# Performance work log

Measured on AMD Instinct MI355X. Metric: run time of the kernel, lower is better.

The kernel has to match this reference:

```python
import jax, jax.numpy as jnp
import numpy as np

B, F_NODES, E = 1024, 128, 1024   # graphs, nodes/graph, edges/graph
H, HEADS = 128, 4
HD = H // HEADS


def setup_inputs() -> dict:
    key = jax.random.key(0)
    ks = jax.random.split(key, 24)
    f32 = jnp.float32
    n = jax.random.normal
    d = {
        "x": n(ks[0], (B, F_NODES), f32),
        "edge_index": jax.random.randint(ks[1], (2, E), 0, F_NODES, dtype=jnp.int32),
        # input projection Linear(1, H)
        "w_in": n(ks[2], (1, H), f32) * 0.5,
        "b_in": n(ks[3], (H,), f32) * 0.02,
        # GAT layer 0: heads=4, concat=True, per-head dim HD
        "gat0_w": n(ks[4], (H, H), f32) * (1.0 / np.sqrt(H)),
        "gat0_as": n(ks[5], (HEADS, HD), f32) * 0.1,
        "gat0_ad": n(ks[6], (HEADS, HD), f32) * 0.1,
        "gat0_b": n(ks[7], (H,), f32) * 0.02,
        "bn0_g": 1.0 + 0.1 * n(ks[8], (H,), f32),
        "bn0_b": 0.1 * n(ks[9], (H,), f32),
        "bn0_m": 0.1 * n(ks[10], (H,), f32),
        "bn0_v": 1.0 + 0.1 * jax.random.uniform(ks[11], (H,), f32),
        # GAT layer 1: heads=1, concat=False
        "gat1_w": n(ks[12], (H, H), f32) * (1.0 / np.sqrt(H)),
        "gat1_as": n(ks[13], (1, H), f32) * 0.1,
        "gat1_ad": n(ks[14], (1, H), f32) * 0.1,
        "gat1_b": n(ks[15], (H,), f32) * 0.02,
        "bn1_g": 1.0 + 0.1 * n(ks[16], (H,), f32),
        "bn1_b": 0.1 * n(ks[17], (H,), f32),
        "bn1_m": 0.1 * n(ks[18], (H,), f32),
        "bn1_v": 1.0 + 0.1 * jax.random.uniform(ks[19], (H,), f32),
        # classifier MLP H -> H//2 -> 1
        "w1": n(ks[20], (H, H // 2), f32) * (1.0 / np.sqrt(H)),
        "b1": n(ks[21], (H // 2,), f32) * 0.02,
        "w2": n(ks[22], (H // 2, 1), f32) * (1.0 / np.sqrt(H // 2)),
        "b2": n(ks[23], (1,), f32) * 0.02,
    }
    return d


def _gat(h, src, dst, N, W, a_s, a_d, b, concat):
    # PyG GATConv (shared lin for src/dst, leaky_relu slope 0.2, softmax over dst)
    heads, hd = a_s.shape
    xh = (h @ W).reshape(N, heads, hd)                      # [N, heads, hd]
    e = jax.nn.leaky_relu(
        jnp.sum(xh * a_s[None], -1)[src] + jnp.sum(xh * a_d[None], -1)[dst],
        0.2,
    )                                                        # [Etot, heads]
    m = jax.ops.segment_max(e, dst, num_segments=N)
    ex = jnp.exp(e - m[dst])
    s = jax.ops.segment_sum(ex, dst, num_segments=N)
    alpha = ex / s[dst]
    out = jax.ops.segment_sum(xh[src] * alpha[..., None], dst, num_segments=N)
    out = out.reshape(N, heads * hd) if concat else out[:, 0]
    return out + b


def _bn(h, g, b, m, v):
    return (h - m) / jnp.sqrt(v + 1e-5) * g + b


def reference(x, edge_index, w_in, b_in,
              gat0_w, gat0_as, gat0_ad, gat0_b, bn0_g, bn0_b, bn0_m, bn0_v,
              gat1_w, gat1_as, gat1_ad, gat1_b, bn1_g, bn1_b, bn1_m, bn1_v,
              w1, b1, w2, b2):
    Bsz, Fn = x.shape
    N = Bsz * Fn
    h = jax.nn.relu(x.reshape(N, 1) @ w_in + b_in)           # [N, H]
    # replicate per-graph edges with node offsets, then add self loops
    offs = jnp.arange(Bsz, dtype=edge_index.dtype) * Fn
    eib = (edge_index[:, None, :] + offs[None, :, None]).reshape(2, -1)
    loops = jnp.arange(N, dtype=edge_index.dtype)
    src = jnp.concatenate([eib[0], loops])
    dst = jnp.concatenate([eib[1], loops])
    h = _gat(h, src, dst, N, gat0_w, gat0_as, gat0_ad, gat0_b, True)
    h = jax.nn.relu(_bn(h, bn0_g, bn0_b, bn0_m, bn0_v))
    h = _gat(h, src, dst, N, gat1_w, gat1_as, gat1_ad, gat1_b, False)
    h = jax.nn.relu(_bn(h, bn1_g, bn1_b, bn1_m, bn1_v))
    # global mean pool (each graph has exactly Fn nodes)
    hp = h.reshape(Bsz, Fn, -1).mean(axis=1)                 # [B, H]
    z = jax.nn.relu(hp @ w1 + b1)
    return z @ w2 + b2                                       # [B, 1]
```

## Files before the change

### kernel.cpp

```cpp
#include <hip/hip_runtime.h>

#define FN   128
#define HDIM 128
#define NH   4
#define HSZ  32
#define EB   1024
#define ET   1152
#define RSW  132

typedef __attribute__((ext_vector_type(8))) short bf16x8;
typedef __attribute__((ext_vector_type(4))) float f32x4;
typedef unsigned int u32;
typedef unsigned short u16;

union U8 { bf16x8 v; u32 u[4]; };

__device__ __forceinline__ u32 pack_hl(float v) {
  const u32 u = __float_as_uint(v);
  const u32 hib = u & 0xFFFF0000u;
  const float lo = v - __uint_as_float(hib);
  return hib | (__float_as_uint(lo) >> 16);
}
__device__ __forceinline__ float unpack_val(u32 p) {
  return __uint_as_float(p & 0xFFFF0000u) + __uint_as_float(p << 16);
}

__device__ __forceinline__ void unpack_frag(const u32* __restrict__ q,
                                            bf16x8& hi, bf16x8& lo)
{
  const uint4 p0 = *(const uint4*)(q);
  const uint4 p1 = *(const uint4*)(q + 4);
  U8 H, L;
  H.u[0] = (p0.x >> 16) | (p0.y & 0xFFFF0000u);
  L.u[0] = (p0.x & 0xFFFFu) | (p0.y << 16);
  H.u[1] = (p0.z >> 16) | (p0.w & 0xFFFF0000u);
  L.u[1] = (p0.z & 0xFFFFu) | (p0.w << 16);
  H.u[2] = (p1.x >> 16) | (p1.y & 0xFFFF0000u);
  L.u[2] = (p1.x & 0xFFFFu) | (p1.y << 16);
  H.u[3] = (p1.z >> 16) | (p1.w & 0xFFFF0000u);
  L.u[3] = (p1.z & 0xFFFFu) | (p1.w << 16);
  hi = H.v; lo = L.v;
}

__device__ __forceinline__ void mfma_gemm(const u32* __restrict__ shl,
                                          float* __restrict__ sg,
                                          const float* __restrict__ W, int t)
{
  const int w = t >> 6, lane = t & 63;
  const int cg = w & 3, rh = w >> 2;
  const int m = lane & 15, quad = lane >> 4;
  const int n0 = cg * 32;

  f32x4 acc[2][2];
  #pragma unroll
  for (int s = 0; s < 2; ++s)
    #pragma unroll
    for (int ct = 0; ct < 2; ++ct) acc[s][ct] = (f32x4){0.f, 0.f, 0.f, 0.f};

  const u32* ap0 = shl + (rh * 32 + m) * RSW + quad * 8;
  const u32* ap1 = shl + (rh * 32 + 16 + m) * RSW + quad * 8;

  #pragma unroll
  for (int kc = 0; kc < 4; ++kc) {
    bf16x8 bhi[2], blo[2];
    #pragma unroll
    for (int ct = 0; ct < 2; ++ct) {
      const int n = n0 + ct * 16 + m;
      float wv[8];
      #pragma unroll
      for (int j = 0; j < 8; ++j) wv[j] = W[(kc * 32 + quad * 8 + j) * HDIM + n];
      U8 Hh, Ll;
      #pragma unroll
      for (int p = 0; p < 4; ++p) {
        const u32 u0 = __float_as_uint(wv[2 * p]);
        const u32 u1 = __float_as_uint(wv[2 * p + 1]);
        const u32 h0 = u0 & 0xFFFF0000u, h1 = u1 & 0xFFFF0000u;
        const float l0 = wv[2 * p]     - __uint_as_float(h0);
        const float l1 = wv[2 * p + 1] - __uint_as_float(h1);
        Hh.u[p] = (u0 >> 16) | h1;
        Ll.u[p] = (__float_as_uint(l0) >> 16) | (__float_as_uint(l1) & 0xFFFF0000u);
      }
      bhi[ct] = Hh.v; blo[ct] = Ll.v;
    }
    bf16x8 a0hi, a0lo, a1hi, a1lo;
    unpack_frag(ap0 + kc * 32, a0hi, a0lo);
    unpack_frag(ap1 + kc * 32, a1hi, a1lo);
    #pragma unroll
    for (int ct = 0; ct < 2; ++ct) {
      acc[0][ct] = __builtin_amdgcn_mfma_f32_16x16x32_bf16(a0hi, bhi[ct], acc[0][ct], 0, 0, 0);
      acc[0][ct] = __builtin_amdgcn_mfma_f32_16x16x32_bf16(a0lo, bhi[ct], acc[0][ct], 0, 0, 0);
      acc[0][ct] = __builtin_amdgcn_mfma_f32_16x16x32_bf16(a0hi, blo[ct], acc[0][ct], 0, 0, 0);
      acc[1][ct] = __builtin_amdgcn_mfma_f32_16x16x32_bf16(a1hi, bhi[ct], acc[1][ct], 0, 0, 0);
      acc[1][ct] = __builtin_amdgcn_mfma_f32_16x16x32_bf16(a1lo, bhi[ct], acc[1][ct], 0, 0, 0);
      acc[1][ct] = __builtin_amdgcn_mfma_f32_16x16x32_bf16(a1hi, blo[ct], acc[1][ct], 0, 0, 0);
    }
  }
  #pragma unroll
  for (int s = 0; s < 2; ++s) {
    const int row0 = rh * 32 + s * 16 + quad * 4;
    #pragma unroll
    for (int ct = 0; ct < 2; ++ct)
      #pragma unroll
      for (int r = 0; r < 4; ++r)
        sg[(row0 + r) * RSW + n0 + ct * 16 + m] = acc[s][ct][r];
  }
}

__global__ __launch_bounds__(1024) void gnn_fused_kernel(
    const float* __restrict__ x, const int* __restrict__ ei,
    const float* __restrict__ w_in, const float* __restrict__ b_in,
    const float* __restrict__ g0w, const float* __restrict__ g0as,
    const float* __restrict__ g0ad, const float* __restrict__ g0b,
    const float* __restrict__ bn0g, const float* __restrict__ bn0b,
    const float* __restrict__ bn0m, const float* __restrict__ bn0v,
    const float* __restrict__ g1w, const float* __restrict__ g1as,
    const float* __restrict__ g1ad, const float* __restrict__ g1b,
    const float* __restrict__ bn1g, const float* __restrict__ bn1b,
    const float* __restrict__ bn1m, const float* __restrict__ bn1v,
    const float* __restrict__ w1, const float* __restrict__ b1,
    const float* __restrict__ w2, const float* __restrict__ b2,
    float* __restrict__ out)
{
  __shared__ u32   shl[FN * RSW];
  __shared__ float sg[FN * RSW];
  __shared__ float s_alpha[NH * ET];
  __shared__ int   s_src[ET];
  __shared__ int   s_rp[FN + 1];
  __shared__ float s_es[512];
  __shared__ float s_ed[512];

  const int t = threadIdx.x;
  const int b = blockIdx.x;

  int* s_deg  = (int*)s_alpha;
  int* s_fill = s_deg + 128;
  const int e_dst = ei[EB + t];
  const int e_src = ei[t];
  if (t < 2 * FN) s_deg[t] = 0;
  __syncthreads();
  atomicAdd(&s_deg[e_dst], 1);

  {
    const int j = t & 127, q = t >> 7;
    const float wv = w_in[j], bv = b_in[j];
    for (int n = q * 16; n < q * 16 + 16; ++n) {
      const float v = fmaxf(fmaf(x[(size_t)b * FN + n], wv, bv), 0.f);
      shl[n * RSW + j] = pack_hl(v);
    }
  }
  __syncthreads();
  if (t < 64) {
    const int v0 = s_deg[2 * t] + 1, v1 = s_deg[2 * t + 1] + 1;
    const int p = v0 + v1;
    int sc = p;
    #pragma unroll
    for (int off = 1; off < 64; off <<= 1) {
      const int o = __shfl_up(sc, off, 64);
      if (t >= off) sc += o;
    }
    s_rp[2 * t] = sc - p;
    s_rp[2 * t + 1] = sc - v1;
    if (t == 63) s_rp[128] = sc;
  }
  __syncthreads();
  {
    const int p = s_rp[e_dst] + atomicAdd(&s_fill[e_dst], 1);
    s_src[p] = e_src;
  }
  if (t < FN) s_src[s_rp[t + 1] - 1] = t;
  __syncthreads();

  mfma_gemm(shl, sg, g0w, t);
  __syncthreads();

  if (t < 512) {
    const int hh = t >> 7, n = t & 127;
    const float* row = sg + n * RSW + hh * HSZ;
    float accs = 0.f, accd = 0.f;
    #pragma unroll
    for (int s = 0; s < 8; ++s) {
      const int d = ((n + s) & 7) * 4;
      const float4 v  = *(const float4*)(row + d);
      const float4 as = *(const float4*)(g0as + hh * HSZ + d);
      const float4 ad = *(const float4*)(g0ad + hh * HSZ + d);
      accs += v.x*as.x + v.y*as.y + v.z*as.z + v.w*as.w;
      accd += v.x*ad.x + v.y*ad.y + v.z*ad.z + v.w*ad.w;
    }
    s_es[hh * 128 + n] = accs;
    s_ed[hh * 128 + n] = accd;
  }
  __syncthreads();

  if (t < 512) {
    const int hh = t >> 7, n = t & 127;
    const float edv = s_ed[hh * 128 + n];
    const int e0 = s_rp[n], e1 = s_rp[n + 1];
    float mv = -1e30f;
    int e = e0;
    for (; e + 2 <= e1; e += 2) {
      const int sA = s_src[e], sB = s_src[e + 1];
      float vA = s_es[hh * 128 + sA] + edv;
      float vB = s_es[hh * 128 + sB] + edv;
      vA = (vA > 0.f) ? vA : 0.2f * vA;
      vB = (vB > 0.f) ? vB : 0.2f * vB;
      s_alpha[hh * ET + e] = vA;
      s_alpha[hh * ET + e + 1] = vB;
      mv = fmaxf(mv, fmaxf(vA, vB));
    }
    if (e < e1) {
      float vA = s_es[hh * 128 + s_src[e]] + edv;
      vA = (vA > 0.f) ? vA : 0.2f * vA;
      s_alpha[hh * ET + e] = vA;
      mv = fmaxf(mv, vA);
    }
    float sum = 0.f;
    e = e0;
    for (; e + 2 <= e1; e += 2) {
      const float exA = __expf(s_alpha[hh * ET + e] - mv);
      const float exB = __expf(s_alpha[hh * ET + e + 1] - mv);
      s_alpha[hh * ET + e] = exA;
      s_alpha[hh * ET + e + 1] = exB;
      sum += exA + exB;
    }
    if (e < e1) {
      const float exA = __expf(s_alpha[hh * ET + e] - mv);
      s_alpha[hh * ET + e] = exA;
      sum += exA;
    }
    s_ed[hh * 128 + n] = 1.f / sum;
  }
  __syncthreads();

  {
    const int cg = t & 15, rg = t >> 4;
    const int c0 = cg * 4, c1 = 64 + cg * 4;
    const int hhA = cg >> 3, hhB = 2 + (cg >> 3);
    const float4 bbA = *(const float4*)&g0b[c0],  bbB = *(const float4*)&g0b[c1];
    const float4 bmA = *(const float4*)&bn0m[c0], bmB = *(const float4*)&bn0m[c1];
    const float4 bvA = *(const float4*)&bn0v[c0], bvB = *(const float4*)&bn0v[c1];
    const float4 bgA = *(const float4*)&bn0g[c0], bgB = *(const float4*)&bn0g[c1];
    const float4 btA = *(const float4*)&bn0b[c0], btB = *(const float4*)&bn0b[c1];
    const float g0_ = bgA.x * rsqrtf(bvA.x + 1e-5f), g1_ = bgA.y * rsqrtf(bvA.y + 1e-5f);
    const float g2_ = bgA.z * rsqrtf(bvA.z + 1e-5f), g3_ = bgA.w * rsqrtf(bvA.w + 1e-5f);
    const float g4_ = bgB.x * rsqrtf(bvB.x + 1e-5f), g5_ = bgB.y * rsqrtf(bvB.y + 1e-5f);
    const float g6_ = bgB.z * rsqrtf(bvB.z + 1e-5f), g7_ = bgB.w * rsqrtf(bvB.w + 1e-5f);
    #pragma unroll
    for (int h2 = 0; h2 < 2; ++h2) {
      const int n = rg + h2 * 64;
      const int e0 = s_rp[n], e1 = s_rp[n + 1];
      const float rsvA = s_ed[hhA * 128 + n];
      const float rsvB = s_ed[hhB * 128 + n];
      float4 a0 = make_float4(0.f, 0.f, 0.f, 0.f);
      float4 a1 = make_float4(0.f, 0.f, 0.f, 0.f);
      for (int e = e0; e < e1; ++e) {
        const int s = s_src[e];
        const float alA = s_alpha[hhA * ET + e];
        const float alB = s_alpha[hhB * ET + e];
        const float4 v0 = *(const float4*)(sg + s * RSW + c0);
        const float4 v1 = *(const float4*)(sg + s * RSW + c1);
        a0.x = fmaf(alA, v0.x, a0.x); a0.y = fmaf(alA, v0.y, a0.y);
        a0.z = fmaf(alA, v0.z, a0.z); a0.w = fmaf(alA, v0.w, a0.w);
        a1.x = fmaf(alB, v1.x, a1.x); a1.y = fmaf(alB, v1.y, a1.y);
        a1.z = fmaf(alB, v1.z, a1.z); a1.w = fmaf(alB, v1.w, a1.w);
      }
      uint4 p0, p1;
      p0.x = pack_hl(fmaxf((a0.x * rsvA + bbA.x - bmA.x) * g0_ + btA.x, 0.f));
      p0.y = pack_hl(fmaxf((a0.y * rsvA + bbA.y - bmA.y) * g1_ + btA.y, 0.f));
      p0.z = pack_hl(fmaxf((a0.z * rsvA + bbA.z - bmA.z) * g2_ + btA.z, 0.f));
      p0.w = pack_hl(fmaxf((a0.w * rsvA + bbA.w - bmA.w) * g3_ + btA.w, 0.f));
      p1.x = pack_hl(fmaxf((a1.x * rsvB + bbB.x - bmB.x) * g4_ + btB.x, 0.f));
      p1.y = pack_hl(fmaxf((a1.y * rsvB + bbB.y - bmB.y) * g5_ + btB.y, 0.f));
      p1.z = pack_hl(fmaxf((a1.z * rsvB + bbB.z - bmB.z) * g6_ + btB.z, 0.f));
      p1.w = pack_hl(fmaxf((a1.w * rsvB + bbB.w - bmB.w) * g7_ + btB.w, 0.f));
      *(uint4*)(shl + n * RSW + c0) = p0;
      *(uint4*)(shl + n * RSW + c1) = p1;
    }
  }
  __syncthreads();

  mfma_gemm(shl, sg, g1w, t);
  __syncthreads();

  if (t < FN) {
    const int n = t;
    const float* row = sg + n * RSW;
    float accs = 0.f, accd = 0.f;
    #pragma unroll 8
    for (int s = 0; s < 32; ++s) {
      const int d = ((n + s) & 31) * 4;
      const float4 v  = *(const float4*)(row + d);
      const float4 as = *(const float4*)(g1as + d);
      const float4 ad = *(const float4*)(g1ad + d);
      accs += v.x*as.x + v.y*as.y + v.z*as.z + v.w*as.w;
      accd += v.x*ad.x + v.y*ad.y + v.z*ad.z + v.w*ad.w;
    }
    s_es[n] = accs;
    s_ed[n] = accd;
  }
  __syncthreads();

  if (t < FN) {
    const int n = t;
    const float edv = s_ed[n];
    const int e0 = s_rp[n], e1 = s_rp[n + 1];
    float mv = -1e30f;
    int e = e0;
    for (; e + 2 <= e1; e += 2) {
      const int sA = s_src[e], sB = s_src[e + 1];
      float vA = s_es[sA] + edv;
      float vB = s_es[sB] + edv;
      vA = (vA > 0.f) ? vA : 0.2f * vA;
      vB = (vB > 0.f) ? vB : 0.2f * vB;
      s_alpha[e] = vA;
      s_alpha[e + 1] = vB;
      mv = fmaxf(mv, fmaxf(vA, vB));
    }
    if (e < e1) {
      float vA = s_es[s_src[e]] + edv;
      vA = (vA > 0.f) ? vA : 0.2f * vA;
      s_alpha[e] = vA;
      mv = fmaxf(mv, vA);
    }
    float sum = 0.f;
    e = e0;
    for (; e + 2 <= e1; e += 2) {
      const float exA = __expf(s_alpha[e] - mv);
      const float exB = __expf(s_alpha[e + 1] - mv);
      s_alpha[e] = exA;
      s_alpha[e + 1] = exB;
      sum += exA + exB;
    }
    if (e < e1) {
      const float exA = __expf(s_alpha[e] - mv);
      s_alpha[e] = exA;
      sum += exA;
    }
    s_ed[n] = 1.f / sum;
  }
  __syncthreads();

  {
    const int cg = t & 15, rg = t >> 4;
    const int c0 = cg * 4, c1 = 64 + cg * 4;
    const float4 bbA = *(const float4*)&g1b[c0],  bbB = *(const float4*)&g1b[c1];
    const float4 bmA = *(const float4*)&bn1m[c0], bmB = *(const float4*)&bn1m[c1];
    const float4 bvA = *(const float4*)&bn1v[c0], bvB = *(const float4*)&bn1v[c1];
    const float4 bgA = *(const float4*)&bn1g[c0], bgB = *(const float4*)&bn1g[c1];
    const float4 btA = *(const float4*)&bn1b[c0], btB = *(const float4*)&bn1b[c1];
    const float g0_ = bgA.x * rsqrtf(bvA.x + 1e-5f), g1_ = bgA.y * rsqrtf(bvA.y + 1e-5f);
    const float g2_ = bgA.z * rsqrtf(bvA.z + 1e-5f), g3_ = bgA.w * rsqrtf(bvA.w + 1e-5f);
    const float g4_ = bgB.x * rsqrtf(bvB.x + 1e-5f), g5_ = bgB.y * rsqrtf(bvB.y + 1e-5f);
    const float g6_ = bgB.z * rsqrtf(bvB.z + 1e-5f), g7_ = bgB.w * rsqrtf(bvB.w + 1e-5f);
    #pragma unroll
    for (int h2 = 0; h2 < 2; ++h2) {
      const int n = rg + h2 * 64;
      const int e0 = s_rp[n], e1 = s_rp[n + 1];
      const float rsv = s_ed[n];
      float4 a0 = make_float4(0.f, 0.f, 0.f, 0.f);
      float4 a1 = make_float4(0.f, 0.f, 0.f, 0.f);
      for (int e = e0; e < e1; ++e) {
        const int s = s_src[e];
        const float al = s_alpha[e];
        const float4 v0 = *(const float4*)(sg + s * RSW + c0);
        const float4 v1 = *(const float4*)(sg + s * RSW + c1);
        a0.x = fmaf(al, v0.x, a0.x); a0.y = fmaf(al, v0.y, a0.y);
        a0.z = fmaf(al, v0.z, a0.z); a0.w = fmaf(al, v0.w, a0.w);
        a1.x = fmaf(al, v1.x, a1.x); a1.y = fmaf(al, v1.y, a1.y);
        a1.z = fmaf(al, v1.z, a1.z); a1.w = fmaf(al, v1.w, a1.w);
      }
      uint4 p0, p1;
      p0.x = pack_hl(fmaxf((a0.x * rsv + bbA.x - bmA.x) * g0_ + btA.x, 0.f));
      p0.y = pack_hl(fmaxf((a0.y * rsv + bbA.y - bmA.y) * g1_ + btA.y, 0.f));
      p0.z = pack_hl(fmaxf((a0.z * rsv + bbA.z - bmA.z) * g2_ + btA.z, 0.f));
      p0.w = pack_hl(fmaxf((a0.w * rsv + bbA.w - bmA.w) * g3_ + btA.w, 0.f));
      p1.x = pack_hl(fmaxf((a1.x * rsv + bbB.x - bmB.x) * g4_ + btB.x, 0.f));
      p1.y = pack_hl(fmaxf((a1.y * rsv + bbB.y - bmB.y) * g5_ + btB.y, 0.f));
      p1.z = pack_hl(fmaxf((a1.z * rsv + bbB.z - bmB.z) * g6_ + btB.z, 0.f));
      p1.w = pack_hl(fmaxf((a1.w * rsv + bbB.w - bmB.w) * g7_ + btB.w, 0.f));
      *(uint4*)(shl + n * RSW + c0) = p0;
      *(uint4*)(shl + n * RSW + c1) = p1;
    }
  }
  __syncthreads();

  float* s_red = s_alpha;
  {
    const int j = t & 127, q = t >> 7;
    float p = 0.f;
    for (int n = q * 16; n < q * 16 + 16; ++n) p += unpack_val(shl[n * RSW + j]);
    s_red[q * 128 + j] = p;
  }
  __syncthreads();
  if (t < FN) {
    float p = 0.f;
    #pragma unroll
    for (int q = 0; q < 8; ++q) p += s_red[q * 128 + t];
    s_es[t] = p * (1.f / 128.f);
  }
  __syncthreads();
  if (t < 512) {
    const int j = t & 63, part = t >> 6;
    float a = 0.f;
    #pragma unroll
    for (int k = part * 16; k < part * 16 + 16; ++k)
      a = fmaf(s_es[k], w1[k * 64 + j], a);
    s_ed[part * 64 + j] = a;
  }
  __syncthreads();
  if (t < 64) {
    float a = b1[t];
    #pragma unroll
    for (int p = 0; p < 8; ++p) a += s_ed[p * 64 + t];
    a = fmaxf(a, 0.f);
    float v = a * w2[t];
    #pragma unroll
    for (int off = 32; off > 0; off >>= 1) v += __shfl_down(v, off, 64);
    if (t == 0) out[b] = v + b2[0];
  }
}

extern "C" void kernel_launch(void* const* d_in, const int* in_sizes, int n_in,
                              void* d_out, int out_size, void* d_ws, size_t ws_size,
                              hipStream_t stream)
{
  const float* x    = (const float*)d_in[0];
  const int*   ei   = (const int*)d_in[1];
  const float* w_in = (const float*)d_in[2];
  const float* b_in = (const float*)d_in[3];
  const float* g0w  = (const float*)d_in[4];
  const float* g0as = (const float*)d_in[5];
  const float* g0ad = (const float*)d_in[6];
  const float* g0b  = (const float*)d_in[7];
  const float* bn0g = (const float*)d_in[8];
  const float* bn0b = (const float*)d_in[9];
  const float* bn0m = (const float*)d_in[10];
  const float* bn0v = (const float*)d_in[11];
  const float* g1w  = (const float*)d_in[12];
  const float* g1as = (const float*)d_in[13];
  const float* g1ad = (const float*)d_in[14];
  const float* g1b  = (const float*)d_in[15];
  const float* bn1g = (const float*)d_in[16];
  const float* bn1b = (const float*)d_in[17];
  const float* bn1m = (const float*)d_in[18];
  const float* bn1v = (const float*)d_in[19];
  const float* w1   = (const float*)d_in[20];
  const float* b1   = (const float*)d_in[21];
  const float* w2   = (const float*)d_in[22];
  const float* b2   = (const float*)d_in[23];

  gnn_fused_kernel<<<1024, 1024, 0, stream>>>(x, ei, w_in, b_in,
      g0w, g0as, g0ad, g0b, bn0g, bn0b, bn0m, bn0v,
      g1w, g1as, g1ad, g1b, bn1g, bn1b, bn1m, bn1v,
      w1, b1, w2, b2, (float*)d_out);
}
```

Measured before the change: 214.0 us.

## Fuse attention logits into GEMM epilogue and parallelize edge softmax without max

Attention logit dot products are now computed directly from MFMA accumulators with cross-lane shuffles, so the separate pass that re-read the projected features from shared memory goes away. Edge scores are computed and exponentiated in parallel over all edges, with the destination packed into the source index. The per-node serial max/exp/sum loops are replaced by a sum folded into the aggregation loop. Dropping the max subtraction risks overflow in exp when logits are large.

Result: slower. 226.5 us (+5.8%).

```diff
diff --git a/kernel.cpp b/kernel.cpp
--- a/kernel.cpp
+++ b/kernel.cpp
@@ -11,7 +11,6 @@
 typedef __attribute__((ext_vector_type(8))) short bf16x8;
 typedef __attribute__((ext_vector_type(4))) float f32x4;
 typedef unsigned int u32;
-typedef unsigned short u16;
 
 union U8 { bf16x8 v; u32 u[4]; };
 
@@ -42,16 +41,31 @@
   hi = H.v; lo = L.v;
 }
 
-__device__ __forceinline__ void mfma_gemm(const u32* __restrict__ shl,
-                                          float* __restrict__ sg,
-                                          const float* __restrict__ W, int t)
+__device__ __forceinline__ void split8(const float* w, bf16x8& hi, bf16x8& lo)
+{
+  U8 H, L;
+  #pragma unroll
+  for (int p = 0; p < 4; ++p) {
+    const u32 u0 = __float_as_uint(w[2 * p]);
+    const u32 u1 = __float_as_uint(w[2 * p + 1]);
+    const u32 h0 = u0 & 0xFFFF0000u, h1 = u1 & 0xFFFF0000u;
+    const float l0 = w[2 * p]     - __uint_as_float(h0);
+    const float l1 = w[2 * p + 1] - __uint_as_float(h1);
+    H.u[p] = (u0 >> 16) | h1;
+    L.u[p] = (__float_as_uint(l0) >> 16) | (__float_as_uint(l1) & 0xFFFF0000u);
+  }
+  hi = H.v; lo = L.v;
+}
+
+__device__ __forceinline__ void mfma_gemm_acc(const u32* __restrict__ shl,
+                                              const float* __restrict__ W,
+                                              int t, f32x4 acc[2][2])
 {
   const int w = t >> 6, lane = t & 63;
   const int cg = w & 3, rh = w >> 2;
   const int m = lane & 15, quad = lane >> 4;
   const int n0 = cg * 32;
 
-  f32x4 acc[2][2];
   #pragma unroll
   for (int s = 0; s < 2; ++s)
     #pragma unroll
@@ -69,18 +83,7 @@
       float wv[8];
       #pragma unroll
       for (int j = 0; j < 8; ++j) wv[j] = W[(kc * 32 + quad * 8 + j) * HDIM + n];
-      U8 Hh, Ll;
-      #pragma unroll
-      for (int p = 0; p < 4; ++p) {
-        const u32 u0 = __float_as_uint(wv[2 * p]);
-        const u32 u1 = __float_as_uint(wv[2 * p + 1]);
-        const u32 h0 = u0 & 0xFFFF0000u, h1 = u1 & 0xFFFF0000u;
-        const float l0 = wv[2 * p]     - __uint_as_float(h0);
-        const float l1 = wv[2 * p + 1] - __uint_as_float(h1);
-        Hh.u[p] = (u0 >> 16) | h1;
-        Ll.u[p] = (__float_as_uint(l0) >> 16) | (__float_as_uint(l1) & 0xFFFF0000u);
-      }
-      bhi[ct] = Hh.v; blo[ct] = Ll.v;
+      split8(wv, bhi[ct], blo[ct]);
     }
     bf16x8 a0hi, a0lo, a1hi, a1lo;
     unpack_frag(ap0 + kc * 32, a0hi, a0lo);
@@ -95,6 +98,14 @@
       acc[1][ct] = __builtin_amdgcn_mfma_f32_16x16x32_bf16(a1hi, blo[ct], acc[1][ct], 0, 0, 0);
     }
   }
+}
+
+__device__ __forceinline__ void store_acc(float* __restrict__ sg, int t,
+                                          const f32x4 acc[2][2])
+{
+  const int w = t >> 6, lane = t & 63;
+  const int cg = w & 3, rh = w >> 2;
+  const int m = lane & 15, quad = lane >> 4;
   #pragma unroll
   for (int s = 0; s < 2; ++s) {
     const int row0 = rh * 32 + s * 16 + quad * 4;
@@ -102,7 +113,45 @@
     for (int ct = 0; ct < 2; ++ct)
       #pragma unroll
       for (int r = 0; r < 4; ++r)
-        sg[(row0 + r) * RSW + n0 + ct * 16 + m] = acc[s][ct][r];
+        sg[(row0 + r) * RSW + cg * 32 + ct * 16 + m] = acc[s][ct][r];
+  }
+}
+
+__device__ __forceinline__ void wave_logits(const float* __restrict__ as_,
+                                            const float* __restrict__ ad_,
+                                            float* __restrict__ es,
+                                            float* __restrict__ ed,
+                                            int t, const f32x4 acc[2][2])
+{
+  const int w = t >> 6, lane = t & 63;
+  const int cg = w & 3, rh = w >> 2;
+  const int li = lane & 15, quad = lane >> 4;
+  const float was0 = as_[cg * 32 + li],      wad0 = ad_[cg * 32 + li];
+  const float was1 = as_[cg * 32 + 16 + li], wad1 = ad_[cg * 32 + 16 + li];
+  float pes[8], ped[8];
+  #pragma unroll
+  for (int s = 0; s < 2; ++s)
+    #pragma unroll
+    for (int r = 0; r < 4; ++r) {
+      pes[s * 4 + r] = acc[s][0][r] * was0 + acc[s][1][r] * was1;
+      ped[s * 4 + r] = acc[s][0][r] * wad0 + acc[s][1][r] * wad1;
+    }
+  #pragma unroll
+  for (int msk = 1; msk < 16; msk <<= 1)
+    #pragma unroll
+    for (int i = 0; i < 8; ++i) {
+      pes[i] += __shfl_xor(pes[i], msk, 64);
+      ped[i] += __shfl_xor(ped[i], msk, 64);
+    }
+  if (li == 0) {
+    #pragma unroll
+    for (int s = 0; s < 2; ++s)
+      #pragma unroll
+      for (int r = 0; r < 4; ++r) {
+        const int row = rh * 32 + s * 16 + quad * 4 + r;
+        es[cg * 128 + row] = pes[s * 4 + r];
+        ed[cg * 128 + row] = ped[s * 4 + r];
+      }
   }
 }
 
@@ -131,6 +180,7 @@
 
   const int t = threadIdx.x;
   const int b = blockIdx.x;
+  f32x4 acc[2][2];
 
   int* s_deg  = (int*)s_alpha;
   int* s_fill = s_deg + 128;
@@ -165,69 +215,32 @@
   __syncthreads();
   {
     const int p = s_rp[e_dst] + atomicAdd(&s_fill[e_dst], 1);
-    s_src[p] = e_src;
-  }
-  if (t < FN) s_src[s_rp[t + 1] - 1] = t;
-  __syncthreads();
-
-  mfma_gemm(shl, sg, g0w, t);
-  __syncthreads();
-
-  if (t < 512) {
-    const int hh = t >> 7, n = t & 127;
-    const float* row = sg + n * RSW + hh * HSZ;
-    float accs = 0.f, accd = 0.f;
-    #pragma unroll
-    for (int s = 0; s < 8; ++s) {
-      const int d = ((n + s) & 7) * 4;
-      const float4 v  = *(const float4*)(row + d);
-      const float4 as = *(const float4*)(g0as + hh * HSZ + d);
-      const float4 ad = *(const float4*)(g0ad + hh * HSZ + d);
-      accs += v.x*as.x + v.y*as.y + v.z*as.z + v.w*as.w;
-      accd += v.x*ad.x + v.y*ad.y + v.z*ad.z + v.w*ad.w;
-    }
-    s_es[hh * 128 + n] = accs;
-    s_ed[hh * 128 + n] = accd;
-  }
-  __syncthreads();
-
-  if (t < 512) {
-    const int hh = t >> 7, n = t & 127;
-    const float edv = s_ed[hh * 128 + n];
-    const int e0 = s_rp[n], e1 = s_rp[n + 1];
-    float mv = -1e30f;
-    int e = e0;
-    for (; e + 2 <= e1; e += 2) {
-      const int sA = s_src[e], sB = s_src[e + 1];
-      float vA = s_es[hh * 128 + sA] + edv;
-      float vB = s_es[hh * 128 + sB] + edv;
-      vA = (vA > 0.f) ? vA : 0.2f * vA;
-      vB = (vB > 0.f) ? vB : 0.2f * vB;
-      s_alpha[hh * ET + e] = vA;
-      s_alpha[hh * ET + e + 1] = vB;
-      mv = fmaxf(mv, fmaxf(vA, vB));
-    }
-    if (e < e1) {
-      float vA = s_es[hh * 128 + s_src[e]] + edv;
-      vA = (vA > 0.f) ? vA : 0.2f * vA;
-      s_alpha[hh * ET + e] = vA;
-      mv = fmaxf(mv, vA);
-    }
-    float sum = 0.f;
-    e = e0;
-    for (; e + 2 <= e1; e += 2) {
-      const float exA = __expf(s_alpha[hh * ET + e] - mv);
-      const float exB = __expf(s_alpha[hh * ET + e + 1] - mv);
-      s_alpha[hh * ET + e] = exA;
-      s_alpha[hh * ET + e + 1] = exB;
-      sum += exA + exB;
-    }
-    if (e < e1) {
-      const float exA = __expf(s_alpha[hh * ET + e] - mv);
-      s_alpha[hh * ET + e] = exA;
-      sum += exA;
-    }
-    s_ed[hh * 128 + n] = 1.f / sum;
+    s_src[p] = e_src | (e_dst << 8);
+  }
+  if (t < FN) s_src[s_rp[t + 1] - 1] = t | (t << 8);
+  __syncthreads();
+
+  mfma_gemm_acc(shl, g0w, t, acc);
+  store_acc(sg, t, acc);
+  wave_logits(g0as, g0ad, s_es, s_ed, t, acc);
+  __syncthreads();
+
+  {
+    #pragma unroll
+    for (int i = t; i < NH * EB; i += 1024) {
+      const int h = i >> 10, e = i & 1023;
+      const int sd = s_src[e];
+      float v = s_es[h * 128 + (sd & 127)] + s_ed[h * 128 + (sd >> 8)];
+      v = (v > 0.f) ? v : 0.2f * v;
+      s_alpha[h * ET + e] = __expf(v);
+    }
+    if (t < 512) {
+      const int h = t >> 7, e = EB + (t & 127);
+      const int sd = s_src[e];
+      float v = s_es[h * 128 + (sd & 127)] + s_ed[h * 128 + (sd >> 8)];
+      v = (v > 0.f) ? v : 0.2f * v;
+      s_alpha[h * ET + e] = __expf(v);
+    }
   }
   __syncthreads();
 
@@ -248,12 +261,16 @@
     for (int h2 = 0; h2 < 2; ++h2) {
       const int n = rg + h2 * 64;
       const int e0 = s_rp[n], e1 = s_rp[n + 1];
-      const float rsvA = s_ed[hhA * 128 + n];
-      const float rsvB = s_ed[hhB * 128 + n];
+      float sumA = 0.f, sumB = 0.f;
+      for (int e = e0; e < e1; ++e) {
+        sumA += s_alpha[hhA * ET + e];
+        sumB += s_alpha[hhB * ET + e];
+      }
+      const float rsvA = 1.f / sumA, rsvB = 1.f / sumB;
       float4 a0 = make_float4(0.f, 0.f, 0.f, 0.f);
       float4 a1 = make_float4(0.f, 0.f, 0.f, 0.f);
       for (int e = e0; e < e1; ++e) {
-        const int s = s_src[e];
+        const int s = s_src[e] & 127;
         const float alA = s_alpha[hhA * ET + e];
         const float alB = s_alpha[hhB * ET + e];
         const float4 v0 = *(const float4*)(sg + s * RSW + c0);
@@ -278,64 +295,24 @@
   }
   __syncthreads();
 
-  mfma_gemm(shl, sg, g1w, t);
-  __syncthreads();
-
-  if (t < FN) {
-    const int n = t;
-    const float* row = sg + n * RSW;
-    float accs = 0.f, accd = 0.f;
-    #pragma unroll 8
-    for (int s = 0; s < 32; ++s) {
-      const int d = ((n + s) & 31) * 4;
-      const float4 v  = *(const float4*)(row + d);
-      const float4 as = *(const float4*)(g1as + d);
-      const float4 ad = *(const float4*)(g1ad + d);
-      accs += v.x*as.x + v.y*as.y + v.z*as.z + v.w*as.w;
-      accd += v.x*ad.x + v.y*ad.y + v.z*ad.z + v.w*ad.w;
-    }
-    s_es[n] = accs;
-    s_ed[n] = accd;
-  }
-  __syncthreads();
-
-  if (t < FN) {
-    const int n = t;
-    const float edv = s_ed[n];
-    const int e0 = s_rp[n], e1 = s_rp[n + 1];
-    float mv = -1e30f;
-    int e = e0;
-    for (; e + 2 <= e1; e += 2) {
-      const int sA = s_src[e], sB = s_src[e + 1];
-      float vA = s_es[sA] + edv;
-      float vB = s_es[sB] + edv;
-      vA = (vA > 0.f) ? vA : 0.2f * vA;
-      vB = (vB > 0.f) ? vB : 0.2f * vB;
-      s_alpha[e] = vA;
-      s_alpha[e + 1] = vB;
-      mv = fmaxf(mv, fmaxf(vA, vB));
-    }
-    if (e < e1) {
-      float vA = s_es[s_src[e]] + edv;
-      vA = (vA > 0.f) ? vA : 0.2f * vA;
-      s_alpha[e] = vA;
-      mv = fmaxf(mv, vA);
-    }
-    float sum = 0.f;
-    e = e0;
-    for (; e + 2 <= e1; e += 2) {
-      const float exA = __expf(s_alpha[e] - mv);
-      const float exB = __expf(s_alpha[e + 1] - mv);
-      s_alpha[e] = exA;
-      s_alpha[e + 1] = exB;
-      sum += exA + exB;
-    }
-    if (e < e1) {
-      const float exA = __expf(s_alpha[e] - mv);
-      s_alpha[e] = exA;
-      sum += exA;
-    }
-    s_ed[n] = 1.f / sum;
+  mfma_gemm_acc(shl, g1w, t, acc);
+  store_acc(sg, t, acc);
+  wave_logits(g1as, g1ad, s_es, s_ed, t, acc);
+  __syncthreads();
+
+  if (t < 128) {
+    s_es[t] = s_es[t] + s_es[t + 128] + s_es[t + 256] + s_es[t + 384];
+  } else if (t < 256) {
+    const int n = t - 128;
+    s_ed[n] = s_ed[n] + s_ed[n + 128] + s_ed[n + 256] + s_ed[n + 384];
+  }
+  __syncthreads();
+
+  for (int i = t; i < ET; i += 1024) {
+    const int sd = s_src[i];
+    float v = s_es[sd & 127] + s_ed[sd >> 8];
+    v = (v > 0.f) ? v : 0.2f * v;
+    s_alpha[i] = __expf(v);
   }
   __syncthreads();
 
@@ -355,11 +332,13 @@
     for (int h2 = 0; h2 < 2; ++h2) {
       const int n = rg + h2 * 64;
       const int e0 = s_rp[n], e1 = s_rp[n + 1];
-      const float rsv = s_ed[n];
+      float sum = 0.f;
+      for (int e = e0; e < e1; ++e) sum += s_alpha[e];
+      const float rsv = 1.f / sum;
       float4 a0 = make_float4(0.f, 0.f, 0.f, 0.f);
       float4 a1 = make_float4(0.f, 0.f, 0.f, 0.f);
       for (int e = e0; e < e1; ++e) {
-        const int s = s_src[e];
+        const int s = s_src[e] & 127;
         const float al = s_alpha[e];
         const float4 v0 = *(const float4*)(sg + s * RSW + c0);
         const float4 v1 = *(const float4*)(sg + s * RSW + c1);
```
